# Performance work log

Measured on AMD Instinct MI355X. Metric: run time of the kernel, lower is better.

## Reference

```python
import jax, jax.numpy as jnp
import numpy as np

B1, B2, R, L, D, H = 48, 48, 36, 30, 1024, 4
EPS = 1e-8


def _l2norm(x):
    return x / (jnp.sqrt(jnp.sum(x * x, axis=-1, keepdims=True)) + EPS)


def _summary_attn(x, w1, b1, w2, b2):
    # x: (B1,B2,N,D). MLP scores -> softmax over N -> weighted mean over H heads.
    h = jax.nn.relu(jnp.einsum('abnd,ed->abne', x, w1) + b1)
    s = jnp.einsum('abne,he->abnh', h, w2) + b2          # (B1,B2,N,H)
    p = jax.nn.softmax(jnp.swapaxes(s, -1, -2), axis=-1)  # (B1,B2,H,N)
    w = jnp.einsum('abhn,abnd->abhd', p, x)               # (B1,B2,H,D)
    return w.mean(axis=-2)                                # (B1,B2,D)


def setup_inputs() -> dict:
    key = jax.random.key(0)
    ks = jax.random.split(key, 12)
    r = np.sqrt(6.0) / np.sqrt(D + D)  # xavier uniform as in init_weights
    return {
        'v1': jax.random.normal(ks[0], (B1, R, D), dtype=jnp.float32),
        'v2': jax.random.normal(ks[1], (B2, L, D), dtype=jnp.float32),
        'w_img': jax.random.uniform(ks[2], (D, D), jnp.float32, -r, r),
        'w_txt': jax.random.uniform(ks[3], (D, D), jnp.float32, -r, r),
        'w1a': jax.random.normal(ks[4], (D, D), jnp.float32) * 0.02,
        'b1a': jnp.zeros((D,), jnp.float32),
        'w2a': jax.random.normal(ks[5], (H, D), jnp.float32) * 0.02,
        'b2a': jnp.zeros((H,), jnp.float32),
        'w1b': jax.random.normal(ks[6], (D, D), jnp.float32) * 0.02,
        'b1b': jnp.zeros((D,), jnp.float32),
        'w2b': jax.random.normal(ks[7], (H, D), jnp.float32) * 0.02,
        'b2b': jnp.zeros((H,), jnp.float32),
    }


def reference(v1, v2, w_img, w_txt, w1a, b1a, w2a, b2a, w1b, b1b, w2b, b2b):
    d = v1.shape[-1]
    inv_sqrt_d = np.float32(1.0 / np.sqrt(d))
    k1 = jnp.einsum('ard,ed->are', v1, w_img)  # (B1,R,D)
    k2 = jnp.einsum('bld,ed->ble', v2, w_txt)  # (B2,L,D)

    # qkv_attention(k2, k1, v1): queries=words, keys/values=regions
    s1 = jnp.einsum('bld,ard->ablr', k2, k1) * inv_sqrt_d   # (B1,B2,L,R)
    p1 = jax.nn.softmax(s1, axis=-1)
    fused_v2 = jnp.einsum('ablr,ard->abld', p1, v1)         # weighted_v1 -> fused_v2

    # qkv_attention(k1, k2, v2): queries=regions, keys/values=words
    s2 = jnp.einsum('ard,bld->abrl', k1, k2) * inv_sqrt_d   # (B1,B2,R,L)
    p2 = jax.nn.softmax(s2, axis=-1)
    fused_v1 = jnp.einsum('abrl,bld->abrd', p2, v2)         # weighted_v2 -> fused_v1

    co_v1 = _l2norm(_summary_attn(fused_v1, w1a, b1a, w2a, b2a))
    co_v2 = _l2norm(_summary_attn(fused_v2, w1b, b1b, w2b, b2b))
    return jnp.sum(co_v1 * co_v2, axis=-1)  # (B1,B2) score matrix
```

## Files before the change

kernel.cpp:

```cpp
#include <hip/hip_runtime.h>

#define D 1024
#define NB1 48
#define NB2 48
#define RR 36
#define LL 30
#define NH 4

typedef short bf16x8 __attribute__((ext_vector_type(8)));
typedef float f32x4 __attribute__((ext_vector_type(4)));
typedef float f32x2 __attribute__((ext_vector_type(2)));
typedef unsigned short u16x8 __attribute__((ext_vector_type(8)));

#define MFMA16(a, b, c) __builtin_amdgcn_mfma_f32_16x16x32_bf16(a, b, c, 0, 0, 0)

__device__ __forceinline__ unsigned short f2bf(float x) {
  unsigned u = __float_as_uint(x);
  u += 0x7FFF + ((u >> 16) & 1);
  return (unsigned short)(u >> 16);
}
__device__ __forceinline__ float bf2f(unsigned short h) {
  return __uint_as_float(((unsigned)h) << 16);
}
__device__ __forceinline__ void split8(const float* v, bf16x8& h8, bf16x8& l8) {
  u16x8 hi, lo;
#pragma unroll
  for (int i = 0; i < 8; ++i) {
    unsigned short h = f2bf(v[i]);
    hi[i] = h;
    lo[i] = f2bf(v[i] - bf2f(h));
  }
  h8 = __builtin_bit_cast(bf16x8, hi);
  l8 = __builtin_bit_cast(bf16x8, lo);
}
__device__ __forceinline__ f32x2 shflx2(f32x2 v, int m) {
  double d = __builtin_bit_cast(double, v);
  d = __shfl_xor(d, m);
  return __builtin_bit_cast(f32x2, d);
}

__device__ __forceinline__ void conv_body(const float* __restrict__ X,
                                          unsigned short* __restrict__ out,
                                          int rows, int g) {
  const int lane = threadIdx.x & 63;
  const int tile = g >> 5, kc = g & 31;
  const int row = tile * 16 + (lane & 15);
  const int k = kc * 32 + (lane >> 4) * 8;
  float v[8];
  if (row < rows) {
    const float4* s = (const float4*)(X + (size_t)row * 1024 + k);
    float4 x0 = s[0], x1 = s[1];
    v[0] = x0.x; v[1] = x0.y; v[2] = x0.z; v[3] = x0.w;
    v[4] = x1.x; v[5] = x1.y; v[6] = x1.z; v[7] = x1.w;
  } else {
#pragma unroll
    for (int i = 0; i < 8; ++i) v[i] = 0.f;
  }
  bf16x8 hi, lo;
  split8(v, hi, lo);
  bf16x8* o = (bf16x8*)(out + (size_t)g * 1024 + lane * 8);
  o[0] = hi;
  o[64] = lo;
}

__global__ __launch_bounds__(256) void conv6(
    const float* __restrict__ v1, const float* __restrict__ v2,
    const float* __restrict__ wimg, const float* __restrict__ wtxt,
    const float* __restrict__ w1a, const float* __restrict__ w1b,
    const float* __restrict__ w2a, const float* __restrict__ w2b,
    unsigned short* v1f, unsigned short* v2f, unsigned short* wimgf,
    unsigned short* wtxtf, unsigned short* w1af, unsigned short* w1bf,
    float4* __restrict__ w2at, float4* __restrict__ w2bt) {
  if (blockIdx.y == 0 && blockIdx.x < 4) {
    int col = blockIdx.x * 256 + threadIdx.x;
    w2at[col] = make_float4(w2a[col], w2a[1024 + col], w2a[2048 + col], w2a[3072 + col]);
    w2bt[col] = make_float4(w2b[col], w2b[1024 + col], w2b[2048 + col], w2b[3072 + col]);
  }
  const float* X; unsigned short* O; int rows;
  switch (blockIdx.y) {
    case 0: X = v1; O = v1f; rows = 1728; break;
    case 1: X = v2; O = v2f; rows = 1440; break;
    case 2: X = wimg; O = wimgf; rows = 1024; break;
    case 3: X = wtxt; O = wtxtf; rows = 1024; break;
    case 4: X = w1a; O = w1af; rows = 1024; break;
    default: X = w1b; O = w1bf; rows = 1024; break;
  }
  const int tiles = (rows + 15) >> 4;
  const int g = blockIdx.x * 4 + (threadIdx.x >> 6);
  if (g >= tiles * 32) return;
  conv_body(X, O, rows, g);
}

__global__ __launch_bounds__(256) void convKG(
    const float* __restrict__ k1, const float* __restrict__ k2,
    const float* __restrict__ G2a, const float* __restrict__ G1b,
    unsigned short* k1f, unsigned short* k2f,
    unsigned short* G2aF, unsigned short* G1bF) {
  const int t = threadIdx.x, lane = t & 63;
  const int y = blockIdx.y;
  if (y < 2) {
    const float* X = y ? k2 : k1;
    unsigned short* O = y ? k2f : k1f;
    const int rows = y ? 1440 : 1728;
    const int tiles = (rows + 15) >> 4;
    const int g = blockIdx.x * 4 + (t >> 6);
    if (g >= tiles * 32) return;
    conv_body(X, O, rows, g);
    return;
  }
  if (blockIdx.x >= 768) return;
  const int bb = blockIdx.x >> 4;
  const int nt = ((blockIdx.x & 15) << 2) + (t >> 6);
  const int c = lane & 15, q = lane >> 4;
  if (y == 2) {
    float v[8];
#pragma unroll
    for (int j = 0; j < 8; ++j) {
      int l = q * 8 + j;
      v[j] = (l < LL) ? G2a[(size_t)(bb * LL + l) * D + nt * 16 + c] : 0.f;
    }
    bf16x8 hi, lo;
    split8(v, hi, lo);
    bf16x8* o = (bf16x8*)(G2aF + ((size_t)(bb * 64 + nt) * 2) * 512 + lane * 8);
    o[0] = hi;
    o[64] = lo;
  } else {
#pragma unroll
    for (int kc = 0; kc < 2; ++kc) {
      float v[8];
#pragma unroll
      for (int j = 0; j < 8; ++j) {
        int r = kc * 32 + q * 8 + j;
        v[j] = (r < RR) ? G1b[(size_t)(bb * RR + r) * D + nt * 16 + c] : 0.f;
      }
      bf16x8 hi, lo;
      split8(v, hi, lo);
      bf16x8* o = (bf16x8*)(G1bF + (((size_t)(bb * 64 + nt) * 2 + kc) * 2) * 512 + lane * 8);
      o[0] = hi;
      o[64] = lo;
    }
  }
}

#define LOAD_FRAGS(AH, AL, BH, BL)                                              \
  {                                                                             \
    _Pragma("unroll") for (int i = 0; i < 4; ++i) {                             \
      AH[i] = Af[ab[i]]; AL[i] = Af[ab[i] + 64]; ab[i] += 128;                  \
    }                                                                           \
    _Pragma("unroll") for (int j = 0; j < 4; ++j) {                             \
      BH[j] = Bf[bb[j]]; BL[j] = Bf[bb[j] + 64]; bb[j] += 128;                  \
    }                                                                           \
  }

#define MFMA_SET(AH, AL, BH, BL)                                                \
  _Pragma("unroll") for (int i = 0; i < 4; ++i)                                 \
      _Pragma("unroll") for (int j = 0; j < 4; ++j) {                           \
    acc[i][j] = MFMA16(AH[i], BH[j], acc[i][j]);                                \
    acc[i][j] = MFMA16(AL[i], BH[j], acc[i][j]);                                \
    acc[i][j] = MFMA16(AH[i], BL[j], acc[i][j]);                                \
  }

__device__ __forceinline__ void gemm2w_body(const bf16x8* __restrict__ Af,
                                            const bf16x8* __restrict__ Bf,
                                            float* __restrict__ C,
                                            int M, int N, float scale,
                                            int Mtiles, int Ntiles) {
  const int lane = threadIdx.x & 63;
  const int w = threadIdx.x >> 6;
  const int mb = blockIdx.y * 8 + w * 4;
  const int nb = blockIdx.x * 4;
  int ab[4], bb[4];
#pragma unroll
  for (int i = 0; i < 4; ++i) {
    int tm = mb + i; if (tm > Mtiles - 1) tm = Mtiles - 1;
    ab[i] = tm * 4096 + lane;
    int tn = nb + i; if (tn > Ntiles - 1) tn = Ntiles - 1;
    bb[i] = tn * 4096 + lane;
  }
  f32x4 acc[4][4];
#pragma unroll
  for (int i = 0; i < 4; ++i)
#pragma unroll
    for (int j = 0; j < 4; ++j) acc[i][j] = (f32x4){0.f, 0.f, 0.f, 0.f};

  bf16x8 ahA[4], alA[4], bhA[4], blA[4];
  bf16x8 ahB[4], alB[4], bhB[4], blB[4];
  LOAD_FRAGS(ahA, alA, bhA, blA);
#pragma unroll 1
  for (int kc = 0; kc < 30; kc += 2) {
    LOAD_FRAGS(ahB, alB, bhB, blB);
    MFMA_SET(ahA, alA, bhA, blA);
    LOAD_FRAGS(ahA, alA, bhA, blA);
    MFMA_SET(ahB, alB, bhB, blB);
  }
  LOAD_FRAGS(ahB, alB, bhB, blB);
  MFMA_SET(ahA, alA, bhA, blA);
  MFMA_SET(ahB, alB, bhB, blB);

  const int c16 = lane & 15, q = lane >> 4;
#pragma unroll
  for (int i = 0; i < 4; ++i) {
#pragma unroll
    for (int reg = 0; reg < 4; ++reg) {
      int r = (mb + i) * 16 + q * 4 + reg;
      if (r < M) {
#pragma unroll
        for (int j = 0; j < 4; ++j) {
          int col = (nb + j) * 16 + c16;
          if (col < N) C[(size_t)r * N + col] = acc[i][j][reg] * scale;
        }
      }
    }
  }
}

__global__ __launch_bounds__(128) void proj_fused(
    const bf16x8* __restrict__ v1f, const bf16x8* __restrict__ v2f,
    const bf16x8* __restrict__ wimgf, const bf16x8* __restrict__ wtxtf,
    const bf16x8* __restrict__ w1af, const bf16x8* __restrict__ w1bf,
    float* k1, float* k2, float* G2a, float* G1b) {
  const int z = blockIdx.z;
  const bf16x8* Af = (z == 0 || z == 3) ? v1f : v2f;
  const bf16x8* Bf = (z == 0) ? wimgf : (z == 1) ? wtxtf : (z == 2) ? w1af : w1bf;
  float* C = (z == 0) ? k1 : (z == 1) ? k2 : (z == 2) ? G2a : G1b;
  const int M = (z == 0 || z == 3) ? 1728 : 1440;
  const int Mt = (z == 0 || z == 3) ? 108 : 90;
  if ((int)blockIdx.y * 8 >= Mt) return;
  gemm2w_body(Af, Bf, C, M, 1024, 1.f, Mt, 64);
}

__global__ __launch_bounds__(128) void cross_s(
    const bf16x8* __restrict__ k2f, const bf16x8* __restrict__ k1f,
    float* Sbuf) {
  gemm2w_body(k2f, k1f, Sbuf, 1440, 1728, 0.03125f, 90, 108);
}

__global__ __launch_bounds__(256, 4) void pair_dir(
    const float* __restrict__ Sb,
    const bf16x8* __restrict__ G2aF, const bf16x8* __restrict__ G1bF,
    const float* __restrict__ b1a, const float4* __restrict__ w2at, const float* __restrict__ b2a,
    const float* __restrict__ b1b, const float4* __restrict__ w2bt, const float* __restrict__ b2b,
    float* __restrict__ U1buf, float* __restrict__ U2buf) {
  const int t = threadIdx.x, lane = t & 63, w = t >> 6;
  const int bx = blockIdx.x;
  int a, b, dir;
  if (bx < 576) {
    dir = 0;
    const int lo = bx & 7, i = bx >> 3;
    b = lo + 8 * (i % 6);
    a = (i / 6) * 4 + w;
  } else {
    dir = 1;
    const int bx2 = bx - 576;
    const int lo = bx2 & 7, i = bx2 >> 3;
    a = lo + 8 * (i % 6);
    b = (i / 6) * 4 + w;
  }
  const int c16 = lane & 15, q = lane >> 4;

  union WSM {
    struct { float p2s[48][36]; float sa[48][NH]; float qa[48]; } A;
    struct { float p1s[32][68]; float sbm[32][NH]; float qb[32]; } B;
  };
  __shared__ __align__(16) WSM sm[4];
  WSM& S = sm[w];

  const float* Sab = Sb + (size_t)(b * LL) * 1728 + a * RR;

  if (dir == 0) {
    if (lane < 48) { S.A.p2s[lane][30] = 0.f; S.A.p2s[lane][31] = 0.f; }
    __builtin_amdgcn_sched_barrier(0);
    for (int i = lane; i < LL * RR; i += 64) {
      int l = i / RR, r = i - l * RR;
      S.A.p2s[r][l] = Sab[(size_t)l * 1728 + r];
    }
    __builtin_amdgcn_sched_barrier(0);
    if (lane < RR) {
      const int r = lane;
      float m = -1e30f;
      for (int l = 0; l < LL; ++l) m = fmaxf(m, S.A.p2s[r][l]);
      float s = 0.f;
      for (int l = 0; l < LL; ++l) {
        float e = __expf(S.A.p2s[r][l] - m);
        S.A.p2s[r][l] = e;
        s += e;
      }
      float inv = 1.f / s;
      for (int l = 0; l < LL; ++l) S.A.p2s[r][l] *= inv;
    }
    __builtin_amdgcn_sched_barrier(0);

    bf16x8 pAh[3], pAl[3];
#pragma unroll
    for (int mt = 0; mt < 3; ++mt) {
      float v[8];
      const float* rp = &S.A.p2s[mt * 16 + c16][q * 8];
      float4 x0 = *(const float4*)rp;
      float4 x1 = *(const float4*)(rp + 4);
      v[0] = x0.x; v[1] = x0.y; v[2] = x0.z; v[3] = x0.w;
      v[4] = x1.x; v[5] = x1.y; v[6] = x1.z; v[7] = x1.w;
      split8(v, pAh[mt], pAl[mt]);
    }

    f32x2 sc01[3][4], sc23[3][4];
#pragma unroll
    for (int mt = 0; mt < 3; ++mt)
#pragma unroll
      for (int reg = 0; reg < 4; ++reg) {
        sc01[mt][reg] = (f32x2){0.f, 0.f};
        sc23[mt][reg] = (f32x2){0.f, 0.f};
      }

    const bf16x8* gA = G2aF + (size_t)(b * 64) * 128 + lane;
#pragma unroll 2
    for (int it = 0; it < 64; ++it) {
      const bf16x8* gp = gA + (size_t)it * 128;
      bf16x8 Bh = gp[0], Bl = gp[64];
      const int col = it * 16 + c16;
      float4 wv = w2at[col];
      float bias = b1a[col];
      f32x2 w01 = {wv.x, wv.y}, w23 = {wv.z, wv.w};
#pragma unroll
      for (int mt = 0; mt < 3; ++mt) {
        f32x4 acc = {bias, bias, bias, bias};
        __builtin_amdgcn_s_setprio(1);
        acc = MFMA16(pAh[mt], Bh, acc);
        acc = MFMA16(pAl[mt], Bh, acc);
        acc = MFMA16(pAh[mt], Bl, acc);
        __builtin_amdgcn_s_setprio(0);
#pragma unroll
        for (int reg = 0; reg < 4; ++reg) {
          float hv = fmaxf(acc[reg], 0.f);
          f32x2 hv2 = {hv, hv};
          sc01[mt][reg] += hv2 * w01;
          sc23[mt][reg] += hv2 * w23;
        }
      }
    }
    f32x2 b01 = {b2a[0], b2a[1]}, b23 = {b2a[2], b2a[3]};
#pragma unroll
    for (int mt = 0; mt < 3; ++mt)
#pragma unroll
      for (int reg = 0; reg < 4; ++reg) {
        f32x2 v01 = sc01[mt][reg], v23 = sc23[mt][reg];
#pragma unroll
        for (int m = 1; m <= 8; m <<= 1) {
          v01 += shflx2(v01, m);
          v23 += shflx2(v23, m);
        }
        if (c16 == 0) {
          f32x2* rp = (f32x2*)&S.A.sa[mt * 16 + q * 4 + reg][0];
          rp[0] = v01 + b01;
          rp[1] = v23 + b23;
        }
      }
    __builtin_amdgcn_sched_barrier(0);
    {
      const int h = q, i = c16;
      float x0 = S.A.sa[i][h];
      float x1 = S.A.sa[i + 16][h];
      float x2 = (i < 4) ? S.A.sa[i + 32][h] : -1e30f;
      float m = fmaxf(fmaxf(x0, x1), x2);
      m = fmaxf(m, __shfl_xor(m, 1));
      m = fmaxf(m, __shfl_xor(m, 2));
      m = fmaxf(m, __shfl_xor(m, 4));
      m = fmaxf(m, __shfl_xor(m, 8));
      float e0 = __expf(x0 - m), e1 = __expf(x1 - m);
      float e2 = (i < 4) ? __expf(x2 - m) : 0.f;
      float s = e0 + e1 + e2;
      s += __shfl_xor(s, 1);
      s += __shfl_xor(s, 2);
      s += __shfl_xor(s, 4);
      s += __shfl_xor(s, 8);
      float inv = 0.25f / s;
      float p0 = e0 * inv, p1 = e1 * inv, p2v = e2 * inv;
      p0 += __shfl_xor(p0, 16); p0 += __shfl_xor(p0, 32);
      p1 += __shfl_xor(p1, 16); p1 += __shfl_xor(p1, 32);
      p2v += __shfl_xor(p2v, 16); p2v += __shfl_xor(p2v, 32);
      if (q == 0) {
        S.A.qa[i] = p0;
        S.A.qa[i + 16] = p1;
        if (i < 4) S.A.qa[i + 32] = p2v;
      }
    }
    __builtin_amdgcn_sched_barrier(0);
    if (lane < LL) {
      const int l = lane;
      float x = 0.f;
      for (int r = 0; r < RR; ++r) x = fmaf(S.A.qa[r], S.A.p2s[r][l], x);
      U2buf[((size_t)b * 48 + a) * 32 + l] = x;
    }
  } else {
    {
      float4 z4 = {0.f, 0.f, 0.f, 0.f};
      for (int i = lane; i < 224; i += 64) {
        int r = i / 7, c4 = i - r * 7;
        *(float4*)&S.B.p1s[r][36 + c4 * 4] = z4;
      }
    }
    __builtin_amdgcn_sched_barrier(0);
    for (int i = lane; i < LL * RR; i += 64) {
      int l = i / RR, r = i - l * RR;
      S.B.p1s[l][r] = Sab[(size_t)l * 1728 + r];
    }
    __builtin_amdgcn_sched_barrier(0);
    if (lane < LL) {
      const int l = lane;
      float m = -1e30f;
      for (int r = 0; r < RR; ++r) m = fmaxf(m, S.B.p1s[l][r]);
      float s = 0.f;
      for (int r = 0; r < RR; ++r) {
        float e = __expf(S.B.p1s[l][r] - m);
        S.B.p1s[l][r] = e;
        s += e;
      }
      float inv = 1.f / s;
      for (int r = 0; r < RR; ++r) S.B.p1s[l][r] *= inv;
    }
    __builtin_amdgcn_sched_barrier(0);

    bf16x8 pBh[2][2], pBl[2][2];
#pragma unroll
    for (int mt = 0; mt < 2; ++mt)
#pragma unroll
      for (int kc = 0; kc < 2; ++kc) {
        float v[8];
        const float* rp = &S.B.p1s[mt * 16 + c16][kc * 32 + q * 8];
        float4 x0 = *(const float4*)rp;
        float4 x1 = *(const float4*)(rp + 4);
        v[0] = x0.x; v[1] = x0.y; v[2] = x0.z; v[3] = x0.w;
        v[4] = x1.x; v[5] = x1.y; v[6] = x1.z; v[7] = x1.w;
        split8(v, pBh[mt][kc], pBl[mt][kc]);
      }

    f32x2 sc01[2][4], sc23[2][4];
#pragma unroll
    for (int mt = 0; mt < 2; ++mt)
#pragma unroll
      for (int reg = 0; reg < 4; ++reg) {
        sc01[mt][reg] = (f32x2){0.f, 0.f};
        sc23[mt][reg] = (f32x2){0.f, 0.f};
      }

    const bf16x8* gB = G1bF + (size_t)(a * 64) * 256 + lane;
#pragma unroll 2
    for (int it = 0; it < 64; ++it) {
      const bf16x8* gp = gB + (size_t)it * 256;
      bf16x8 B0h = gp[0], B0l = gp[64], B1h = gp[128], B1l = gp[192];
      const int col = it * 16 + c16;
      float4 wv = w2bt[col];
      float bias = b1b[col];
      f32x2 w01 = {wv.x, wv.y}, w23 = {wv.z, wv.w};
#pragma unroll
      for (int mt = 0; mt < 2; ++mt) {
        f32x4 acc = {bias, bias, bias, bias};
        __builtin_amdgcn_s_setprio(1);
        acc = MFMA16(pBh[mt][0], B0h, acc);
        acc = MFMA16(pBl[mt][0], B0h, acc);
        acc = MFMA16(pBh[mt][0], B0l, acc);
        acc = MFMA16(pBh[mt][1], B1h, acc);
        acc = MFMA16(pBl[mt][1], B1h, acc);
        acc = MFMA16(pBh[mt][1], B1l, acc);
        __builtin_amdgcn_s_setprio(0);
#pragma unroll
        for (int reg = 0; reg < 4; ++reg) {
          float hv = fmaxf(acc[reg], 0.f);
          f32x2 hv2 = {hv, hv};
          sc01[mt][reg] += hv2 * w01;
          sc23[mt][reg] += hv2 * w23;
        }
      }
    }
    f32x2 b01 = {b2b[0], b2b[1]}, b23 = {b2b[2], b2b[3]};
#pragma unroll
    for (int mt = 0; mt < 2; ++mt)
#pragma unroll
      for (int reg = 0; reg < 4; ++reg) {
        f32x2 v01 = sc01[mt][reg], v23 = sc23[mt][reg];
#pragma unroll
        for (int m = 1; m <= 8; m <<= 1) {
          v01 += shflx2(v01, m);
          v23 += shflx2(v23, m);
        }
        if (c16 == 0) {
          f32x2* rp = (f32x2*)&S.B.sbm[mt * 16 + q * 4 + reg][0];
          rp[0] = v01 + b01;
          rp[1] = v23 + b23;
        }
      }
    __builtin_amdgcn_sched_barrier(0);
    {
      const int h = q, i = c16;
      float x0 = S.B.sbm[i][h];
      float x1 = (i < 14) ? S.B.sbm[i + 16][h] : -1e30f;
      float m = fmaxf(x0, x1);
      m = fmaxf(m, __shfl_xor(m, 1));
      m = fmaxf(m, __shfl_xor(m, 2));
      m = fmaxf(m, __shfl_xor(m, 4));
      m = fmaxf(m, __shfl_xor(m, 8));
      float e0 = __expf(x0 - m);
      float e1 = (i < 14) ? __expf(x1 - m) : 0.f;
      float s = e0 + e1;
      s += __shfl_xor(s, 1);
      s += __shfl_xor(s, 2);
      s += __shfl_xor(s, 4);
      s += __shfl_xor(s, 8);
      float inv = 0.25f / s;
      float p0 = e0 * inv, p1 = e1 * inv;
      p0 += __shfl_xor(p0, 16); p0 += __shfl_xor(p0, 32);
      p1 += __shfl_xor(p1, 16); p1 += __shfl_xor(p1, 32);
      if (q == 0) {
        S.B.qb[i] = p0;
        if (i < 14) S.B.qb[i + 16] = p1;
      }
    }
    __builtin_amdgcn_sched_barrier(0);
    if (lane < RR) {
      const int r = lane;
      float x = 0.f;
      for (int l = 0; l < LL; ++l) x = fmaf(S.B.qb[l], S.B.p1s[l][r], x);
      U1buf[((size_t)a * 48 + b) * 40 + r] = x;
    }
  }
}

__global__ __launch_bounds__(256) void y_batch(
    const float* __restrict__ v1, const float* __restrict__ v2,
    const float* __restrict__ U1buf, const float* __restrict__ U2buf,
    float* __restrict__ YA, float* __restrict__ YB) {
  const int bb = blockIdx.x;
  const int col = blockIdx.z * 256 + threadIdx.x;
  __shared__ float us[48 * 40];
  float y[48];
#pragma unroll
  for (int i = 0; i < 48; ++i) y[i] = 0.f;
  if (blockIdx.y == 0) {
    for (int i = threadIdx.x; i < 48 * 32; i += 256) us[i] = U2buf[(size_t)bb * 1536 + i];
    __syncthreads();
    const float* V = v2 + (size_t)bb * LL * 1024 + col;
    for (int l = 0; l < LL; ++l) {
      float v = V[(size_t)l * 1024];
#pragma unroll
      for (int i = 0; i < 48; ++i) y[i] = fmaf(us[i * 32 + l], v, y[i]);
    }
    float* Yo = YA + (size_t)bb * 48 * 1024 + col;
#pragma unroll
    for (int i = 0; i < 48; ++i) Yo[(size_t)i * 1024] = y[i];
  } else {
    for (int i = threadIdx.x; i < 48 * 40; i += 256) us[i] = U1buf[(size_t)bb * 1920 + i];
    __syncthreads();
    const float* V = v1 + (size_t)bb * RR * 1024 + col;
    for (int r = 0; r < RR; ++r) {
      float v = V[(size_t)r * 1024];
#pragma unroll
      for (int i = 0; i < 48; ++i) y[i] = fmaf(us[i * 40 + r], v, y[i]);
    }
    float* Yo = YB + (size_t)bb * 48 * 1024 + col;
#pragma unroll
    for (int i = 0; i < 48; ++i) Yo[(size_t)i * 1024] = y[i];
  }
}

__global__ __launch_bounds__(256) void pair_final(
    const float* __restrict__ YA, const float* __restrict__ YB,
    float* __restrict__ out) {
  const int pair = blockIdx.x;
  const int a = pair / NB2;
  const int b = pair - a * NB2;
  const int t = threadIdx.x;
  const float4* ya = (const float4*)(YA + ((size_t)b * 48 + a) * 1024);
  const float4* yb = (const float4*)(YB + ((size_t)a * 48 + b) * 1024);
  float4 va = ya[t], vb = yb[t];
  float num = va.x * vb.x + va.y * vb.y + va.z * vb.z + va.w * vb.w;
  float n1 = va.x * va.x + va.y * va.y + va.z * va.z + va.w * va.w;
  float n2 = vb.x * vb.x + vb.y * vb.y + vb.z * vb.z + vb.w * vb.w;
#pragma unroll
  for (int off = 32; off; off >>= 1) {
    num += __shfl_down(num, off);
    n1 += __shfl_down(n1, off);
    n2 += __shfl_down(n2, off);
  }
  __shared__ float r3[3][4];
  if ((t & 63) == 0) {
    r3[0][t >> 6] = num; r3[1][t >> 6] = n1; r3[2][t >> 6] = n2;
  }
  __syncthreads();
  if (t == 0) {
    float nu = r3[0][0] + r3[0][1] + r3[0][2] + r3[0][3];
    float s1 = sqrtf(fmaxf(r3[1][0] + r3[1][1] + r3[1][2] + r3[1][3], 0.f));
    float s2 = sqrtf(fmaxf(r3[2][0] + r3[2][1] + r3[2][2] + r3[2][3], 0.f));
    out[pair] = nu / ((s1 + 1e-8f) * (s2 + 1e-8f));
  }
}

extern "C" void kernel_launch(void* const* d_in, const int* in_sizes, int n_in,
                              void* d_out, int out_size, void* d_ws, size_t ws_size,
                              hipStream_t stream) {
  const float* v1    = (const float*)d_in[0];
  const float* v2    = (const float*)d_in[1];
  const float* w_img = (const float*)d_in[2];
  const float* w_txt = (const float*)d_in[3];
  const float* w1a   = (const float*)d_in[4];
  const float* b1a   = (const float*)d_in[5];
  const float* w2a   = (const float*)d_in[6];
  const float* b2a   = (const float*)d_in[7];
  const float* w1b   = (const float*)d_in[8];
  const float* b1b   = (const float*)d_in[9];
  const float* w2b   = (const float*)d_in[10];
  const float* b2b   = (const float*)d_in[11];
  float* out = (float*)d_out;

  float* ws   = (float*)d_ws;
  float* k1   = ws;
  float* k2   = k1 + (size_t)1728 * 1024;
  float* G2a  = k2 + (size_t)1440 * 1024;
  float* G1b  = G2a + (size_t)1440 * 1024;
  float* Sbuf = G1b + (size_t)1728 * 1024;
  float* Cbuf = Sbuf + (size_t)1440 * 1728;
  float* g22  = Cbuf + (size_t)1440 * 1728;
  float* g11  = g22 + (size_t)48 * 900;

  unsigned short* fb    = (unsigned short*)(g11 + (size_t)48 * 1296);
  unsigned short* v1f   = fb;
  unsigned short* v2f   = v1f + (size_t)108 * 32768;
  unsigned short* k1f   = v2f + (size_t)92 * 32768;
  unsigned short* k2f   = k1f + (size_t)108 * 32768;
  unsigned short* wimgf = k2f + (size_t)92 * 32768;
  unsigned short* wtxtf = wimgf + (size_t)64 * 32768;
  unsigned short* w1af  = wtxtf + (size_t)64 * 32768;
  unsigned short* w1bf  = w1af + (size_t)64 * 32768;
  unsigned short* G2aF  = w1bf + (size_t)64 * 32768;
  unsigned short* G1bF  = G2aF + (size_t)48 * 65536;

  float4* w2at = (float4*)g22;
  float4* w2bt = w2at + 1024;

  float* U2buf = G2a;
  float* U1buf = U2buf + (size_t)48 * 48 * 32;
  float* YA = Cbuf;
  float* YB = (float*)k1f;

  conv6<<<dim3(864, 6), 256, 0, stream>>>(v1, v2, w_img, w_txt, w1a, w1b,
                                          w2a, w2b,
                                          v1f, v2f, wimgf, wtxtf, w1af, w1bf,
                                          w2at, w2bt);

  proj_fused<<<dim3(16, 14, 4), 128, 0, stream>>>(
      (const bf16x8*)v1f, (const bf16x8*)v2f, (const bf16x8*)wimgf,
      (const bf16x8*)wtxtf, (const bf16x8*)w1af, (const bf16x8*)w1bf,
      k1, k2, G2a, G1b);

  convKG<<<dim3(864, 4), 256, 0, stream>>>(k1, k2, G2a, G1b,
                                           k1f, k2f, G2aF, G1bF);

  cross_s<<<dim3(27, 12), 128, 0, stream>>>(
      (const bf16x8*)k2f, (const bf16x8*)k1f, Sbuf);

  pair_dir<<<1152, 256, 0, stream>>>(
      Sbuf, (const bf16x8*)G2aF, (const bf16x8*)G1bF,
      b1a, w2at, b2a, b1b, w2bt, b2b, U1buf, U2buf);
  y_batch<<<dim3(48, 2, 4), 256, 0, stream>>>(v1, v2, U1buf, U2buf, YA, YB);
  pair_final<<<2304, 256, 0, stream>>>(YA, YB, out);
}
```

Measured before the change: 286.9 us.

## Fuse bf16 hi/lo split of k1/k2 into projection GEMM epilogue

```diff
diff --git a/kernel.cpp b/kernel.cpp
--- a/kernel.cpp
+++ b/kernel.cpp
@@ -91,28 +91,15 @@
   conv_body(X, O, rows, g);
 }
 
-__global__ __launch_bounds__(256) void convKG(
-    const float* __restrict__ k1, const float* __restrict__ k2,
-    const float* __restrict__ G2a, const float* __restrict__ G1b,
-    unsigned short* k1f, unsigned short* k2f,
-    unsigned short* G2aF, unsigned short* G1bF) {
+__global__ __launch_bounds__(256) void convG(const float* __restrict__ G2a,
+                                             const float* __restrict__ G1b,
+                                             unsigned short* G2aF,
+                                             unsigned short* G1bF) {
   const int t = threadIdx.x, lane = t & 63;
-  const int y = blockIdx.y;
-  if (y < 2) {
-    const float* X = y ? k2 : k1;
-    unsigned short* O = y ? k2f : k1f;
-    const int rows = y ? 1440 : 1728;
-    const int tiles = (rows + 15) >> 4;
-    const int g = blockIdx.x * 4 + (t >> 6);
-    if (g >= tiles * 32) return;
-    conv_body(X, O, rows, g);
-    return;
-  }
-  if (blockIdx.x >= 768) return;
   const int bb = blockIdx.x >> 4;
   const int nt = ((blockIdx.x & 15) << 2) + (t >> 6);
   const int c = lane & 15, q = lane >> 4;
-  if (y == 2) {
+  if (blockIdx.y == 0) {
     float v[8];
 #pragma unroll
     for (int j = 0; j < 8; ++j) {
@@ -160,15 +147,11 @@
     acc[i][j] = MFMA16(AH[i], BL[j], acc[i][j]);                                \
   }
 
-__device__ __forceinline__ void gemm2w_body(const bf16x8* __restrict__ Af,
-                                            const bf16x8* __restrict__ Bf,
-                                            float* __restrict__ C,
-                                            int M, int N, float scale,
-                                            int Mtiles, int Ntiles) {
-  const int lane = threadIdx.x & 63;
-  const int w = threadIdx.x >> 6;
-  const int mb = blockIdx.y * 8 + w * 4;
-  const int nb = blockIdx.x * 4;
+__device__ __forceinline__ void gemm2w_acc(const bf16x8* __restrict__ Af,
+                                           const bf16x8* __restrict__ Bf,
+                                           int Mtiles, int Ntiles,
+                                           int mb, int nb, int lane,
+                                           f32x4 (&acc)[4][4]) {
   int ab[4], bb[4];
 #pragma unroll
   for (int i = 0; i < 4; ++i) {
@@ -177,7 +160,6 @@
     int tn = nb + i; if (tn > Ntiles - 1) tn = Ntiles - 1;
     bb[i] = tn * 4096 + lane;
   }
-  f32x4 acc[4][4];
 #pragma unroll
   for (int i = 0; i < 4; ++i)
 #pragma unroll
@@ -196,7 +178,12 @@
   LOAD_FRAGS(ahB, alB, bhB, blB);
   MFMA_SET(ahA, alA, bhA, blA);
   MFMA_SET(ahB, alB, bhB, blB);
-
+}
+
+__device__ __forceinline__ void gemm2w_store_fp32(f32x4 (&acc)[4][4],
+                                                  float* __restrict__ C,
+                                                  int M, int N, float scale,
+                                                  int mb, int nb, int lane) {
   const int c16 = lane & 15, q = lane >> 4;
 #pragma unroll
   for (int i = 0; i < 4; ++i) {
@@ -218,21 +205,72 @@
     const bf16x8* __restrict__ v1f, const bf16x8* __restrict__ v2f,
     const bf16x8* __restrict__ wimgf, const bf16x8* __restrict__ wtxtf,
     const bf16x8* __restrict__ w1af, const bf16x8* __restrict__ w1bf,
-    float* k1, float* k2, float* G2a, float* G1b) {
+    float* G2a, float* G1b,
+    unsigned short* k1f, unsigned short* k2f) {
   const int z = blockIdx.z;
+  const int lane = threadIdx.x & 63;
+  const int w = threadIdx.x >> 6;
+  const int mb = blockIdx.y * 8 + w * 4;
+  const int nb = blockIdx.x * 4;
   const bf16x8* Af = (z == 0 || z == 3) ? v1f : v2f;
   const bf16x8* Bf = (z == 0) ? wimgf : (z == 1) ? wtxtf : (z == 2) ? w1af : w1bf;
-  float* C = (z == 0) ? k1 : (z == 1) ? k2 : (z == 2) ? G2a : G1b;
-  const int M = (z == 0 || z == 3) ? 1728 : 1440;
   const int Mt = (z == 0 || z == 3) ? 108 : 90;
   if ((int)blockIdx.y * 8 >= Mt) return;
-  gemm2w_body(Af, Bf, C, M, 1024, 1.f, Mt, 64);
+
+  __shared__ __align__(16) float tlds[2][4][16][68];
+
+  f32x4 acc[4][4];
+  gemm2w_acc(Af, Bf, Mt, 64, mb, nb, lane, acc);
+
+  if (z <= 1) {
+    unsigned short* F = z ? k2f : k1f;
+    const int c16 = lane & 15, q = lane >> 4;
+#pragma unroll
+    for (int i = 0; i < 4; ++i)
+#pragma unroll
+      for (int j = 0; j < 4; ++j)
+#pragma unroll
+        for (int reg = 0; reg < 4; ++reg)
+          tlds[w][i][q * 4 + reg][j * 16 + c16] = acc[i][j][reg];
+    __builtin_amdgcn_sched_barrier(0);
+    const int r16 = lane & 15, q2 = lane >> 4;
+#pragma unroll
+    for (int i = 0; i < 4; ++i) {
+      if (mb + i < Mt) {
+#pragma unroll
+        for (int kcl = 0; kcl < 2; ++kcl) {
+          const float* rp = &tlds[w][i][r16][kcl * 32 + q2 * 8];
+          float4 x0 = *(const float4*)rp;
+          float4 x1 = *(const float4*)(rp + 4);
+          float v[8];
+          v[0] = x0.x; v[1] = x0.y; v[2] = x0.z; v[3] = x0.w;
+          v[4] = x1.x; v[5] = x1.y; v[6] = x1.z; v[7] = x1.w;
+          bf16x8 hi, lo;
+          split8(v, hi, lo);
+          size_t g = (size_t)(mb + i) * 32 + (nb >> 1) + kcl;
+          bf16x8* o = (bf16x8*)(F + g * 1024 + lane * 8);
+          o[0] = hi;
+          o[64] = lo;
+        }
+      }
+    }
+  } else {
+    float* C = (z == 2) ? G2a : G1b;
+    const int M = (z == 2) ? 1440 : 1728;
+    gemm2w_store_fp32(acc, C, M, 1024, 1.f, mb, nb, lane);
+  }
 }
 
 __global__ __launch_bounds__(128) void cross_s(
     const bf16x8* __restrict__ k2f, const bf16x8* __restrict__ k1f,
     float* Sbuf) {
-  gemm2w_body(k2f, k1f, Sbuf, 1440, 1728, 0.03125f, 90, 108);
+  const int lane = threadIdx.x & 63;
+  const int w = threadIdx.x >> 6;
+  const int mb = blockIdx.y * 8 + w * 4;
+  const int nb = blockIdx.x * 4;
+  f32x4 acc[4][4];
+  gemm2w_acc(k2f, k1f, 90, 108, mb, nb, lane, acc);
+  gemm2w_store_fp32(acc, Sbuf, 1440, 1728, 0.03125f, mb, nb, lane);
 }
 
 __global__ __launch_bounds__(256, 4) void pair_dir(
@@ -619,6 +657,7 @@
   float* Cbuf = Sbuf + (size_t)1440 * 1728;
   float* g22  = Cbuf + (size_t)1440 * 1728;
   float* g11  = g22 + (size_t)48 * 900;
+  (void)k1; (void)k2;
 
   unsigned short* fb    = (unsigned short*)(g11 + (size_t)48 * 1296);
   unsigned short* v1f   = fb;
@@ -648,13 +687,12 @@
   proj_fused<<<dim3(16, 14, 4), 128, 0, stream>>>(
       (const bf16x8*)v1f, (const bf16x8*)v2f, (const bf16x8*)wimgf,
       (const bf16x8*)wtxtf, (const bf16x8*)w1af, (const bf16x8*)w1bf,
-      k1, k2, G2a, G1b);
-
-  convKG<<<dim3(864, 4), 256, 0, stream>>>(k1, k2, G2a, G1b,
-                                           k1f, k2f, G2aF, G1bF);
+      G2a, G1b, k1f, k2f);
 
   cross_s<<<dim3(27, 12), 128, 0, stream>>>(
       (const bf16x8*)k2f, (const bf16x8*)k1f, Sbuf);
+
+  convG<<<dim3(768, 2), 256, 0, stream>>>(G2a, G1b, G2aF, G1bF);
 
   pair_dir<<<1152, 256, 0, stream>>>(
       Sbuf, (const bf16x8*)G2aF, (const bf16x8*)G1bF,
```

After: 284.1 us. No clear change (-1.0%).
